# Kernel optimization log

Measured on AMD Instinct MI355X. Metric: run time of the kernel, lower is better.

## Reference

```python
import jax, jax.numpy as jnp
import numpy as np

S, B, D, H = 2048, 2, 1024, 16
DK = D // H
SCALE = 1.0 / np.sqrt(DK)


def setup_inputs() -> dict:
    key = jax.random.key(0)
    ks = jax.random.split(key, 12)
    std = 1.0 / np.sqrt(D)
    inp = {
        "query": jax.random.normal(ks[0], (S, B, D), jnp.float32),
        "key": jax.random.normal(ks[1], (S, B, D), jnp.float32),
        "value": jax.random.normal(ks[2], (S, B, D), jnp.float32),
        # causal mask [S, S, 1]; mask[i, j] = 1 iff query i may attend key j
        "mask": jnp.tril(jnp.ones((S, S), jnp.bool_))[:, :, None],
        "Wq": jax.random.normal(ks[3], (D, D), jnp.float32) * std,
        "bq": jax.random.normal(ks[4], (D,), jnp.float32) * std,
        "Wk": jax.random.normal(ks[5], (D, D), jnp.float32) * std,
        "bk": jax.random.normal(ks[6], (D,), jnp.float32) * std,
        "Wv": jax.random.normal(ks[7], (D, D), jnp.float32) * std,
        "bv": jax.random.normal(ks[8], (D,), jnp.float32) * std,
        "Wo": jax.random.normal(ks[9], (D, D), jnp.float32) * std,
        "bo": jax.random.normal(ks[10], (D,), jnp.float32) * std,
    }
    return inp


def _proj(x, W, b):
    # nn.Linear: x @ W.T + b, then split into heads -> [S, B, H, DK]
    s, bsz, _ = x.shape
    y = jnp.einsum('sbd,ed->sbe', x, W) + b
    return y.reshape(s, bsz, H, DK)


def reference(query, key, value, mask, Wq, bq, Wk, bk, Wv, bv, Wo, bo):
    q = _proj(query, Wq, bq)   # [S,B,H,DK]
    k = _proj(key, Wk, bk)
    v = _proj(value, Wv, bv)
    scores = jnp.einsum('ibhd,jbhd->ijbh', q, k) * SCALE  # [S,S,B,H]
    m = mask[:, :, :, None]  # [S,S,1,1] or [S,S,B,1]
    scores = jnp.where(m, scores, jnp.float32(-1e9))
    attn = jax.nn.softmax(scores, axis=1)
    x = jnp.einsum('ijbh,jbhd->ibhd', attn, v)  # [S,B,H,DK]
    x = x.reshape(S, B, D)
    return jnp.einsum('sbd,ed->sbe', x, Wo) + bo
```

## Files before the change

### kernel.cpp

```cpp
#include <hip/hip_runtime.h>
#include <stdint.h>

#define S_LEN 2048
#define BATCH 2
#define DMODEL 1024
#define NHEAD 16
#define DHEAD 64
#define QSCALE 0.18033688011112042f

typedef float f32x4 __attribute__((ext_vector_type(4)));
typedef float f32x16 __attribute__((ext_vector_type(16)));
typedef __bf16 bf16x8 __attribute__((ext_vector_type(8)));
typedef unsigned short u16x8 __attribute__((ext_vector_type(8)));

#if __has_builtin(__builtin_amdgcn_exp2f)
#define EXP2(x) __builtin_amdgcn_exp2f(x)
#else
#define EXP2(x) exp2f(x)
#endif

__device__ __forceinline__ unsigned short f2bf(float f) {
  union { float f; unsigned int u; } v;
  v.f = f;
  unsigned int u = v.u;
  return (unsigned short)((u + 0x7fffu + ((u >> 16) & 1u)) >> 16);
}

__device__ __forceinline__ unsigned pk2(float lo, float hi_) {
  union { __bf16 h[2]; unsigned u; } c;
  c.h[0] = (__bf16)lo; c.h[1] = (__bf16)hi_;
  return c.u;
}

__device__ __forceinline__ void gld16(const void* g, void* l) {
  __builtin_amdgcn_global_load_lds((__attribute__((address_space(1))) void*)(g),
                                   (__attribute__((address_space(3))) void*)(l),
                                   16, 0, 0);
}

__device__ __forceinline__ float xswapf(float x) { return __shfl_xor(x, 32, 64); }
__device__ __forceinline__ unsigned xswapu(unsigned x) {
  return (unsigned)__shfl_xor((int)x, 32, 64);
}

__global__ void cvt_w_kernel(const float* __restrict__ wq, const float* __restrict__ wk,
                             const float* __restrict__ wv, const float* __restrict__ wosrc,
                             unsigned short* __restrict__ wp, unsigned short* __restrict__ wo) {
  const int b = blockIdx.x;
  const int z = b >> 10, local = b & 1023;
  const float* src = (z == 0 ? wq : (z == 1 ? wk : (z == 2 ? wv : wosrc))) + (size_t)local * 1024;
  unsigned short* dst = (z < 3 ? wp + (size_t)z * 1048576 : wo) + (size_t)local * 1024;
  const int i = threadIdx.x * 4;
  const float4 val = *(const float4*)(src + i);
  ushort4 o;
  o.x = f2bf(val.x); o.y = f2bf(val.y); o.z = f2bf(val.z); o.w = f2bf(val.w);
  *(ushort4*)(dst + i) = o;
}

template <int MODE>
__global__ __launch_bounds__(256, 2) void gemm_bt(
    const float* __restrict__ Aq, const float* __restrict__ Akk, const float* __restrict__ Avv,
    const unsigned short* __restrict__ Ab,
    const unsigned short* __restrict__ Wbase,
    const float* __restrict__ bias0, const float* __restrict__ bias1,
    const float* __restrict__ bias2,
    unsigned short* __restrict__ qw, unsigned short* __restrict__ kw,
    unsigned short* __restrict__ vtw, float* __restrict__ outp) {
  constexpr int N = DMODEL;
  constexpr int K = DMODEL;
  constexpr int AST = (MODE == 0) ? 40 : 32;
  __shared__ unsigned short At[128 * AST];
  __shared__ unsigned short Bt[128 * 32];

  const int m0 = blockIdx.x * 128;
  const int n0 = blockIdx.y * 128;
  const int z = (MODE == 0) ? blockIdx.z : 0;
  const unsigned short* W = Wbase + (size_t)z * N * K;
  const float* bias = (z == 0 ? bias0 : (z == 1 ? bias1 : bias2));

  const int tid = threadIdx.x;
  const int w = tid >> 6, l = tid & 63;
  const int wr = w >> 1, wc = w & 1;
  const int lr = l & 15, lg = l >> 4;

  const int srow = tid >> 2;
  const int scol = (tid & 3) * 8;

  const int arow = tid >> 1;
  const int aks = (tid & 1) << 4;
  const float* Af = (MODE == 0) ? (z == 0 ? Aq : (z == 1 ? Akk : Avv)) : nullptr;
  const float* abase = (MODE == 0) ? (Af + (size_t)(m0 + arow) * K + aks) : nullptr;

  float4 av[4];
  if (MODE == 0) {
#pragma unroll
    for (int c = 0; c < 4; ++c) av[c] = *(const float4*)(abase + 4 * c);
  }

  f32x4 acc[4][4] = {};

  for (int k0 = 0; k0 < K; k0 += 32) {
    if (k0) __syncthreads();
    if (MODE == 0) {
      union { __bf16 h[8]; u16x8 v; } c0, c1;
#pragma unroll
      for (int j = 0; j < 4; ++j) { c0.h[j] = (__bf16)av[0][j]; c0.h[4 + j] = (__bf16)av[1][j]; }
#pragma unroll
      for (int j = 0; j < 4; ++j) { c1.h[j] = (__bf16)av[2][j]; c1.h[4 + j] = (__bf16)av[3][j]; }
      *(u16x8*)&At[arow * AST + aks] = c0.v;
      *(u16x8*)&At[arow * AST + aks + 8] = c1.v;
    } else {
      gld16(Ab + (size_t)(m0 + srow) * K + k0 + scol, (char*)At + w * 1024);
      gld16(Ab + (size_t)(m0 + 64 + srow) * K + k0 + scol, (char*)At + w * 1024 + 4096);
    }
    gld16(W + (size_t)(n0 + srow) * K + k0 + scol, (char*)Bt + w * 1024);
    gld16(W + (size_t)(n0 + 64 + srow) * K + k0 + scol, (char*)Bt + w * 1024 + 4096);
    __syncthreads();

    if (MODE == 0 && k0 + 32 < K) {
#pragma unroll
      for (int c = 0; c < 4; ++c) av[c] = *(const float4*)(abase + k0 + 32 + 4 * c);
    }

    bf16x8 af[4], bfr[4];
#pragma unroll
    for (int mt = 0; mt < 4; ++mt)
      af[mt] = *(const bf16x8*)&At[(wr * 64 + mt * 16 + lr) * AST + lg * 8];
#pragma unroll
    for (int nt = 0; nt < 4; ++nt)
      bfr[nt] = *(const bf16x8*)&Bt[(wc * 64 + nt * 16 + lr) * 32 + lg * 8];
#pragma unroll
    for (int mt = 0; mt < 4; ++mt)
#pragma unroll
      for (int nt = 0; nt < 4; ++nt)
        acc[mt][nt] = __builtin_amdgcn_mfma_f32_16x16x32_bf16(af[mt], bfr[nt], acc[mt][nt], 0, 0, 0);
  }

#pragma unroll
  for (int mt = 0; mt < 4; ++mt) {
#pragma unroll
    for (int nt = 0; nt < 4; ++nt) {
#pragma unroll
      for (int r = 0; r < 4; ++r) {
        const int gm = m0 + wr * 64 + mt * 16 + lg * 4 + r;
        const int gn = n0 + wc * 64 + nt * 16 + lr;
        float v = acc[mt][nt][r] + bias[gn];
        if (MODE == 1) {
          outp[(size_t)gm * N + gn] = v;
        } else {
          if (z == 0) v *= QSCALE;
          const int s = gm >> 1, bb = gm & 1;
          const int h = gn >> 6, dk = gn & 63;
          const int bh = bb * NHEAD + h;
          const unsigned short bv_ = f2bf(v);
          if (z == 0)
            qw[((size_t)bh * S_LEN + s) * DHEAD + dk] = bv_;
          else if (z == 1)
            kw[((size_t)bh * S_LEN + s) * DHEAD + dk] = bv_;
          else
            vtw[(((size_t)bh * 32 + (s >> 6)) * 64 + dk) * 64 + (s & 63)] = bv_;
        }
      }
    }
  }
}

__global__ __launch_bounds__(512) void attn_kernel(
    const unsigned short* __restrict__ qw, const unsigned short* __restrict__ kw,
    const unsigned short* __restrict__ vtw, unsigned short* __restrict__ x2) {
  __shared__ unsigned short klds[2][4][4096];
  __shared__ float mlscr[3][2][64][2];

  const int bh = blockIdx.x;
  const int xq = blockIdx.y;
  const int bb = bh >> 4, h = bh & 15;
  const int tid = threadIdx.x;
  const int w = tid >> 6, l = tid & 63;
  const int q5 = l & 31, hi = l >> 5;
  const int quar = w >> 1, wh = w & 1;

  const size_t qkbase = (size_t)bh * S_LEN * DHEAD;

  const int qtA = 31 - xq, qtB = xq;
  const int nA = qtA + 1, nB = qtB + 1;
  const int sA_ = (nA + 3) >> 2;
  const int sTot = sA_ + ((nB + 3) >> 2);

  auto stage = [&](int t0, int lim2, int buf) {
#pragma unroll
    for (int r = 0; r < 4; ++r) {
      const int slot = w * 4 + r;
      const int ti = slot >> 3;
      const int row = ((slot & 7) << 3) + (l >> 3);
      const int ch = (l & 7) ^ (l >> 3);
      int t = t0 + ti;
      if (t >= lim2) t = lim2 - 1;
      gld16(kw + qkbase + (size_t)(t * 64 + row) * DHEAD + ch * 8,
            (char*)klds + buf * 32768 + ti * 8192 + (slot & 7) * 1024);
    }
  };

  int qt = qtA;
  int qrow = qt * 64 + wh * 32 + q5;
  bf16x8 qf[4];
#pragma unroll
  for (int d = 0; d < 4; ++d)
    qf[d] = *(const bf16x8*)&qw[qkbase + (size_t)qrow * DHEAD + d * 16 + hi * 8];

  f32x16 oacc0, oacc1;
#pragma unroll
  for (int r = 0; r < 16; ++r) { oacc0[r] = 0.f; oacc1[r] = 0.f; }
  float mrun = -1e30f, lrun = 0.f;

  stage(0, nA, 0);
  __syncthreads();

  for (int s = 0; s < sTot; ++s) {
    const int cur = s & 1;
    const bool mergeIter = (s == sA_ - 1) || (s == sTot - 1);
    if (!mergeIter) {
      int t0, lim2;
      if (s + 1 < sA_) { t0 = 4 * (s + 1); lim2 = nA; }
      else { t0 = 4 * (s + 1 - sA_); lim2 = nB; }
      stage(t0, lim2, cur ^ 1);
    }

    const bool phA = (s < sA_);
    const int myt = (phA ? 4 * s : 4 * (s - sA_)) + quar;
    const int lim = phA ? nA : nB;

    if (myt < lim) {
      const int kt = myt;
      const char* kb = (const char*)klds + cur * 32768 + quar * 8192;

      const unsigned short* vt = vtw + ((size_t)bh * 32 + kt) * 4096;
      const unsigned short* vrow0 = vt + q5 * 64 + 8 * hi;
      const unsigned short* vrow1 = vt + (32 + q5) * 64 + 8 * hi;
      bf16x8 vf0[4], vf1[4];
      vf0[0] = *(const bf16x8*)(vrow0);
      vf1[0] = *(const bf16x8*)(vrow1);
      vf0[1] = *(const bf16x8*)(vrow0 + 16);
      vf1[1] = *(const bf16x8*)(vrow1 + 16);

      f32x16 scA, scB;
#pragma unroll
      for (int r = 0; r < 16; ++r) { scA[r] = 0.f; scB[r] = 0.f; }
      __builtin_amdgcn_s_setprio(1);
#pragma unroll
      for (int d = 0; d < 4; ++d) {
        const int ch = (2 * d + hi) ^ (q5 & 7);
        const bf16x8 kfA = *(const bf16x8*)(kb + q5 * 128 + ch * 16);
        const bf16x8 kfB = *(const bf16x8*)(kb + (32 + q5) * 128 + ch * 16);
        scA = __builtin_amdgcn_mfma_f32_32x32x16_bf16(kfA, qf[d], scA, 0, 0, 0);
        scB = __builtin_amdgcn_mfma_f32_32x32x16_bf16(kfB, qf[d], scB, 0, 0, 0);
      }
      __builtin_amdgcn_s_setprio(0);

      if (kt == qt) {
        const int qloc = wh * 32 + q5;
#pragma unroll
        for (int r = 0; r < 16; ++r) {
          const int kv = (r & 3) + 8 * (r >> 2) + 4 * hi;
          if (kv > qloc) scA[r] = -1e9f;
          if (kv + 32 > qloc) scB[r] = -1e9f;
        }
      }

      float mx[8];
#pragma unroll
      for (int j = 0; j < 8; ++j)
        mx[j] = fmaxf(fmaxf(scA[j], scA[j + 8]), fmaxf(scB[j], scB[j + 8]));
#pragma unroll
      for (int j = 0; j < 4; ++j) mx[j] = fmaxf(mx[j], mx[j + 4]);
      float tmax = fmaxf(fmaxf(mx[0], mx[1]), fmaxf(mx[2], mx[3]));
      tmax = fmaxf(tmax, xswapf(tmax));
      if (!__all(tmax <= mrun + 8.0f)) {
        const float mnew = fmaxf(mrun, tmax);
        const float resc = EXP2(mrun - mnew);
        mrun = mnew;
        lrun *= resc;
#pragma unroll
        for (int r = 0; r < 16; ++r) { oacc0[r] *= resc; oacc1[r] *= resc; }
      }
#pragma unroll
      for (int r = 0; r < 16; ++r) scA[r] = EXP2(scA[r] - mrun);
#pragma unroll
      for (int r = 0; r < 16; ++r) scB[r] = EXP2(scB[r] - mrun);

      vf0[2] = *(const bf16x8*)(vrow0 + 32);
      vf1[2] = *(const bf16x8*)(vrow1 + 32);
      vf0[3] = *(const bf16x8*)(vrow0 + 48);
      vf1[3] = *(const bf16x8*)(vrow1 + 48);

      float sm[8];
#pragma unroll
      for (int j = 0; j < 8; ++j)
        sm[j] = (scA[j] + scA[j + 8]) + (scB[j] + scB[j + 8]);
#pragma unroll
      for (int j = 0; j < 4; ++j) sm[j] += sm[j + 4];
      float rsum = (sm[0] + sm[1]) + (sm[2] + sm[3]);
      rsum += xswapf(rsum);
      lrun += rsum;

      unsigned pk[2][8];
#pragma unroll
      for (int g = 0; g < 4; ++g) {
        pk[0][2 * g]     = pk2(scA[4 * g],     scA[4 * g + 1]);
        pk[0][2 * g + 1] = pk2(scA[4 * g + 2], scA[4 * g + 3]);
        pk[1][2 * g]     = pk2(scB[4 * g],     scB[4 * g + 1]);
        pk[1][2 * g + 1] = pk2(scB[4 * g + 2], scB[4 * g + 3]);
      }

      __builtin_amdgcn_s_setprio(1);
#pragma unroll
      for (int t = 0; t < 4; ++t) {
        const int c = t >> 1, ks = t & 1;
        const unsigned o0 = pk[c][4 * ks + 0], o1 = pk[c][4 * ks + 1];
        const unsigned o2 = pk[c][4 * ks + 2], o3 = pk[c][4 * ks + 3];
        const unsigned ea = xswapu(hi ? o0 : o2);
        const unsigned eb = xswapu(hi ? o1 : o3);
        union { unsigned u[4]; bf16x8 v; } pb;
        pb.u[0] = hi ? ea : o0;
        pb.u[1] = hi ? eb : o1;
        pb.u[2] = hi ? o2 : ea;
        pb.u[3] = hi ? o3 : eb;
        oacc0 = __builtin_amdgcn_mfma_f32_32x32x16_bf16(vf0[t], pb.v, oacc0, 0, 0, 0);
        oacc1 = __builtin_amdgcn_mfma_f32_32x32x16_bf16(vf1[t], pb.v, oacc1, 0, 0, 0);
      }
      __builtin_amdgcn_s_setprio(0);
    }

    if (mergeIter) {
      __syncthreads();
      float* scr = (float*)klds;
      const int kx = l & 7;
      if (quar != 0) {
        f32x4* d4 = (f32x4*)(scr + (size_t)(((quar - 1) * 2 + wh) * 64 + l) * 32);
#pragma unroll
      for (int c = 0; c < 4; ++c) {
          f32x4 ch_;
#pragma unroll
          for (int j = 0; j < 4; ++j) ch_[j] = oacc0[c * 4 + j];
          d4[c ^ kx] = ch_;
        }
#pragma unroll
        for (int c = 0; c < 4; ++c) {
          f32x4 ch_;
#pragma unroll
          for (int j = 0; j < 4; ++j) ch_[j] = oacc1[c * 4 + j];
          d4[(4 + c) ^ kx] = ch_;
        }
        mlscr[quar - 1][wh][l][0] = mrun;
        mlscr[quar - 1][wh][l][1] = lrun;
      }
      __syncthreads();
      if (quar == 0) {
        float ms = mrun, lm = lrun;
        f32x16 a0 = oacc0, a1 = oacc1;
#pragma unroll
        for (int p = 1; p <= 3; ++p) {
          const f32x4* s4 = (const f32x4*)(scr + (size_t)(((p - 1) * 2 + wh) * 64 + l) * 32);
          const float mp = mlscr[p - 1][wh][l][0], lp = mlscr[p - 1][wh][l][1];
          const float mn = fmaxf(ms, mp);
          const float c0 = EXP2(ms - mn), c1 = EXP2(mp - mn);
#pragma unroll
          for (int g = 0; g < 4; ++g) {
            const f32x4 p0 = s4[g ^ kx];
            const f32x4 p1 = s4[(4 + g) ^ kx];
#pragma unroll
            for (int j = 0; j < 4; ++j) {
              a0[4 * g + j] = a0[4 * g + j] * c0 + p0[j] * c1;
              a1[4 * g + j] = a1[4 * g + j] * c0 + p1[j] * c1;
            }
          }
          lm = lm * c0 + lp * c1;
          ms = mn;
        }
        const float invl = 1.0f / lm;
        const size_t obase = ((size_t)qrow * BATCH + bb) * DMODEL + h * DHEAD;
#pragma unroll
        for (int g = 0; g < 4; ++g) {
          const int d0 = 8 * g + 4 * hi;
          ushort4 s0, s1;
          s0.x = f2bf(a0[4 * g + 0] * invl);
          s0.y = f2bf(a0[4 * g + 1] * invl);
          s0.z = f2bf(a0[4 * g + 2] * invl);
          s0.w = f2bf(a0[4 * g + 3] * invl);
          s1.x = f2bf(a1[4 * g + 0] * invl);
          s1.y = f2bf(a1[4 * g + 1] * invl);
          s1.z = f2bf(a1[4 * g + 2] * invl);
          s1.w = f2bf(a1[4 * g + 3] * invl);
          *(ushort4*)(x2 + obase + d0) = s0;
          *(ushort4*)(x2 + obase + 32 + d0) = s1;
        }
      }
      if (s == sA_ - 1) {
        qt = qtB;
        qrow = qt * 64 + wh * 32 + q5;
#pragma unroll
        for (int d = 0; d < 4; ++d)
          qf[d] = *(const bf16x8*)&qw[qkbase + (size_t)qrow * DHEAD + d * 16 + hi * 8];
#pragma unroll
        for (int r = 0; r < 16; ++r) { oacc0[r] = 0.f; oacc1[r] = 0.f; }
        mrun = -1e30f;
        lrun = 0.f;
      }
      __syncthreads();
      if (s + 1 < sTot) stage(0, nB, cur ^ 1);
    }
    __syncthreads();
  }
}

extern "C" void kernel_launch(void* const* d_in, const int* in_sizes, int n_in,
                              void* d_out, int out_size, void* d_ws, size_t ws_size,
                              hipStream_t stream) {
  (void)in_sizes; (void)n_in; (void)out_size;
  if (ws_size < (size_t)67108864) return;

  const float* query = (const float*)d_in[0];
  const float* key_  = (const float*)d_in[1];
  const float* value = (const float*)d_in[2];
  const float* Wq = (const float*)d_in[4];
  const float* bq = (const float*)d_in[5];
  const float* Wk = (const float*)d_in[6];
  const float* bk = (const float*)d_in[7];
  const float* Wv = (const float*)d_in[8];
  const float* bv = (const float*)d_in[9];
  const float* Wo = (const float*)d_in[10];
  const float* bo = (const float*)d_in[11];

  char* ws = (char*)d_ws;
  unsigned short* wp  = (unsigned short*)(ws);
  unsigned short* wo  = (unsigned short*)(ws + 6291456);
  unsigned short* qws = (unsigned short*)(ws + 8388608);
  unsigned short* kws = (unsigned short*)(ws + 16777216);
  unsigned short* vtw = (unsigned short*)(ws + 25165824);
  unsigned short* x2  = (unsigned short*)(ws + 33554432);

  cvt_w_kernel<<<4096, 256, 0, stream>>>(Wq, Wk, Wv, Wo, wp, wo);

  gemm_bt<0><<<dim3(32, 8, 3), 256, 0, stream>>>(query, key_, value, nullptr, wp,
                                                 bq, bk, bv, qws, kws, vtw, nullptr);
  attn_kernel<<<dim3(32, 16), 512, 0, stream>>>(qws, kws, vtw, x2);
  gemm_bt<1><<<dim3(32, 8, 1), 256, 0, stream>>>(nullptr, nullptr, nullptr, x2, wo,
                                                 bo, bo, bo, nullptr, nullptr, nullptr,
                                                 (float*)d_out);
}
```

Measured before the change: 134.7 us.

## Double-buffer LDS tiles in projection GEMM to overlap loads with MFMA

Gives the A and B shared-memory tiles in the projection/output GEMM two buffers each. The next k-slice is staged while MFMAs run on the current one, leaving one barrier per iteration instead of two. The fp32 A loads are also remapped so each thread reads 4 rows with 4 contiguous floats, and the fp32 register prefetch now runs two slices ahead. This doubles LDS use per block, which may reduce occupancy, and adds register pressure.

```diff
diff --git a/kernel.cpp b/kernel.cpp
--- a/kernel.cpp
+++ b/kernel.cpp
@@ -68,9 +68,10 @@
     unsigned short* __restrict__ vtw, float* __restrict__ outp) {
   constexpr int N = DMODEL;
   constexpr int K = DMODEL;
+  constexpr int NK = K / 32;
   constexpr int AST = (MODE == 0) ? 40 : 32;
-  __shared__ unsigned short At[128 * AST];
-  __shared__ unsigned short Bt[128 * 32];
+  __shared__ unsigned short At[2][128 * AST];
+  __shared__ unsigned short Bt[2][128 * 32];
 
   const int m0 = blockIdx.x * 128;
   const int n0 = blockIdx.y * 128;
@@ -86,54 +87,68 @@
   const int srow = tid >> 2;
   const int scol = (tid & 3) * 8;
 
-  const int arow = tid >> 1;
-  const int aks = (tid & 1) << 4;
+  const int arow8 = tid >> 3;
+  const int acol8 = (tid & 7) * 4;
   const float* Af = (MODE == 0) ? (z == 0 ? Aq : (z == 1 ? Akk : Avv)) : nullptr;
-  const float* abase = (MODE == 0) ? (Af + (size_t)(m0 + arow) * K + aks) : nullptr;
+  const float* abase = (MODE == 0) ? (Af + (size_t)(m0 + arow8) * K + acol8) : nullptr;
 
   float4 av[4];
-  if (MODE == 0) {
-#pragma unroll
-    for (int c = 0; c < 4; ++c) av[c] = *(const float4*)(abase + 4 * c);
-  }
+  auto loadA = [&](int k0) {
+#pragma unroll
+    for (int c = 0; c < 4; ++c)
+      av[c] = *(const float4*)(abase + (size_t)(c * 32) * K + k0);
+  };
+  auto writeA = [&](int buf) {
+#pragma unroll
+    for (int c = 0; c < 4; ++c) {
+      union { __bf16 h[4]; uint2 u; } p;
+#pragma unroll
+      for (int j = 0; j < 4; ++j) p.h[j] = (__bf16)av[c][j];
+      *(uint2*)&At[buf][(c * 32 + arow8) * AST + acol8] = p.u;
+    }
+  };
+  auto stageA_g = [&](int k0, int buf) {
+    gld16(Ab + (size_t)(m0 + srow) * K + k0 + scol, (char*)&At[buf][0] + w * 1024);
+    gld16(Ab + (size_t)(m0 + 64 + srow) * K + k0 + scol, (char*)&At[buf][0] + w * 1024 + 4096);
+  };
+  auto stageB = [&](int k0, int buf) {
+    gld16(W + (size_t)(n0 + srow) * K + k0 + scol, (char*)&Bt[buf][0] + w * 1024);
+    gld16(W + (size_t)(n0 + 64 + srow) * K + k0 + scol, (char*)&Bt[buf][0] + w * 1024 + 4096);
+  };
 
   f32x4 acc[4][4] = {};
 
-  for (int k0 = 0; k0 < K; k0 += 32) {
-    if (k0) __syncthreads();
-    if (MODE == 0) {
-      union { __bf16 h[8]; u16x8 v; } c0, c1;
-#pragma unroll
-      for (int j = 0; j < 4; ++j) { c0.h[j] = (__bf16)av[0][j]; c0.h[4 + j] = (__bf16)av[1][j]; }
-#pragma unroll
-      for (int j = 0; j < 4; ++j) { c1.h[j] = (__bf16)av[2][j]; c1.h[4 + j] = (__bf16)av[3][j]; }
-      *(u16x8*)&At[arow * AST + aks] = c0.v;
-      *(u16x8*)&At[arow * AST + aks + 8] = c1.v;
-    } else {
-      gld16(Ab + (size_t)(m0 + srow) * K + k0 + scol, (char*)At + w * 1024);
-      gld16(Ab + (size_t)(m0 + 64 + srow) * K + k0 + scol, (char*)At + w * 1024 + 4096);
-    }
-    gld16(W + (size_t)(n0 + srow) * K + k0 + scol, (char*)Bt + w * 1024);
-    gld16(W + (size_t)(n0 + 64 + srow) * K + k0 + scol, (char*)Bt + w * 1024 + 4096);
-    __syncthreads();
-
-    if (MODE == 0 && k0 + 32 < K) {
-#pragma unroll
-      for (int c = 0; c < 4; ++c) av[c] = *(const float4*)(abase + k0 + 32 + 4 * c);
+  if (MODE == 0) { loadA(0); writeA(0); loadA(32); }
+  else stageA_g(0, 0);
+  stageB(0, 0);
+  __syncthreads();
+
+  for (int kk = 0; kk < NK; ++kk) {
+    const int cur = kk & 1;
+    if (kk + 1 < NK) {
+      if (MODE == 0) {
+        writeA(cur ^ 1);
+        if (kk + 2 < NK) loadA((kk + 2) * 32);
+      } else {
+        stageA_g((kk + 1) * 32, cur ^ 1);
+      }
+      stageB((kk + 1) * 32, cur ^ 1);
     }
 
     bf16x8 af[4], bfr[4];
 #pragma unroll
     for (int mt = 0; mt < 4; ++mt)
-      af[mt] = *(const bf16x8*)&At[(wr * 64 + mt * 16 + lr) * AST + lg * 8];
+      af[mt] = *(const bf16x8*)&At[cur][(wr * 64 + mt * 16 + lr) * AST + lg * 8];
 #pragma unroll
     for (int nt = 0; nt < 4; ++nt)
-      bfr[nt] = *(const bf16x8*)&Bt[(wc * 64 + nt * 16 + lr) * 32 + lg * 8];
+      bfr[nt] = *(const bf16x8*)&Bt[cur][(wc * 64 + nt * 16 + lr) * 32 + lg * 8];
 #pragma unroll
     for (int mt = 0; mt < 4; ++mt)
 #pragma unroll
       for (int nt = 0; nt < 4; ++nt)
         acc[mt][nt] = __builtin_amdgcn_mfma_f32_16x16x32_bf16(af[mt], bfr[nt], acc[mt][nt], 0, 0, 0);
+
+    __syncthreads();
   }
 
 #pragma unroll
```

Result: no change. 135.6 us (+0.6%).
